# Kernel optimization log

Measured on AMD Instinct MI355X. Metric: run time of the kernel, lower is better.

Reference implementation:

```python
import jax, jax.numpy as jnp
import numpy as np

# Synthetic taxonomy matching BuildDictionaries/Build_H_Matrix structure
N_O, N_F, N_G, N_S = 25, 150, 1200, 4800
PIQUETS = [0, N_O, N_O + N_F, N_O + N_F + N_G, N_O + N_F + N_G + N_S]  # [0,25,175,1375,6175]
C_TOTAL = PIQUETS[-1]
WEIGHTS = [0.25, 0.25, 0.15, 0.1]
E = float(np.e)
BATCH = 4096


def _build_H():
    H = np.zeros((C_TOTAL, C_TOTAL), dtype=np.float32)
    fam = np.arange(N_F)
    H[fam % N_O, PIQUETS[1] + fam] = 1.0              # order -> family
    gen = np.arange(N_G)
    H[PIQUETS[1] + gen % N_F, PIQUETS[2] + gen] = 1.0  # family -> genus
    sp = np.arange(N_S)
    H[PIQUETS[2] + sp % N_G, PIQUETS[3] + sp] = 1.0    # genus -> species
    return H


def setup_inputs() -> dict:
    key = jax.random.key(0)
    k1, k2 = jax.random.split(key)
    H_np = _build_H()
    # parent[j] = i such that H[i, j] == 1 (same as the get_grandparents row scan)
    parent_np = np.argmax(H_np, axis=0).astype(np.int64)
    y_pred = jax.random.normal(k1, (BATCH, C_TOTAL), dtype=jnp.float32)
    y_true = jax.random.randint(k2, (BATCH,), 0, N_S, dtype=jnp.int64)
    return {
        "y_pred": y_pred,
        "y_true": y_true,
        "H": jnp.asarray(H_np),
        "parent": jnp.asarray(parent_np),
    }


def _ce(logits, labels):
    # nn.CrossEntropyLoss with mean reduction
    logp = jax.nn.log_softmax(logits, axis=-1)
    return -jnp.mean(jnp.take_along_axis(logp, labels[:, None], axis=1))


def reference(y_pred, y_true, H, parent):
    nb_levels = 4
    # Per-level logit slices: y_pred[:, piquets[k]:piquets[k+1]]
    lp = [y_pred[:, PIQUETS[k]:PIQUETS[k + 1]] for k in range(nb_levels)]

    # Ancestor chain (vectorized get_grandparents): global ids per level
    g3 = y_true + PIQUETS[3]           # global species id (y_true += piquets[-2])
    g2 = parent[g3]                    # genus
    g1 = parent[g2]                    # family
    g0 = parent[g1]                    # order
    lt = [g0 - PIQUETS[0], g1 - PIQUETS[1], g2 - PIQUETS[2], g3 - PIQUETS[3]]

    # Faithful quirk: argmax indices are LOCAL to each level's slice,
    # and H is indexed with those local indices (as in the original code).
    argm = [jnp.argmax(x, axis=-1) for x in lp]

    s = _ce(lp[0], lt[0])
    loss = jnp.zeros((), dtype=y_pred.dtype)
    for k in range(1, nb_levels):
        h = H[argm[k - 1], argm[k]]                      # [B] gather
        pen = jnp.sum(jnp.where(h == 0, E, 0.0))         # sum_i (H==0)*e
        s = (s + pen + _ce(lp[k], lt[k])) * WEIGHTS[k]   # running sum *= weights[k]
        loss = loss + s
    return loss
```

## Files before the change

### kernel.cpp

```cpp
#include <hip/hip_runtime.h>
#include <math.h>

#define C_TOTAL 6175
#define BATCH 4096
#define NLEV 4

__device__ __constant__ int PIQ[5] = {0, 25, 175, 1375, 6175};

__device__ inline void am_merge(float& m, int& idx, float m2, int i2) {
    const bool take = (m2 > m) || (m2 == m && i2 < idx);
    idx = take ? i2 : idx;
    m   = fmaxf(m, m2);
}

__device__ inline void upd(float x, int i, float& m, float& s, int& ii) {
    s += __expf(fminf(x, 60.f));
    ii = (x > m) ? i : ii;
    m  = fmaxf(m, x);
}

__device__ inline void process_span(const float* __restrict__ p, int W,
                                    int lane, float& S, float& M, int& I) {
    float ms = -INFINITY, ss = 0.f;
    int   is_ = 0x7fffffff;

    int pe = (int)((4u - ((((uintptr_t)p) >> 2) & 3u)) & 3u);
    if (pe > W) pe = W;
    if (lane < pe) {
        const float x = p[lane];
        ss = __expf(fminf(x, 60.f));
        ms = x; is_ = lane;
    }
    const int rem  = W - pe;
    const int nvec = rem >> 2;
    const int tail = rem & 3;
    const float4* vp = reinterpret_cast<const float4*>(p + pe);

    float m0 = -INFINITY, m1 = -INFINITY, m2 = -INFINITY, m3 = -INFINITY;
    float s0 = 0.f, s1 = 0.f, s2 = 0.f, s3 = 0.f;
    int   i0 = 0x1fffffff, i1 = 0x1fffffff, i2 = 0x1fffffff, i3 = 0x1fffffff;

    int i = lane;
    for (; i + 64 < nvec; i += 128) {
        const float4 a = vp[i];
        const float4 b = vp[i + 64];
        upd(a.x, i, m0, s0, i0); upd(a.y, i, m1, s1, i1);
        upd(a.z, i, m2, s2, i2); upd(a.w, i, m3, s3, i3);
        upd(b.x, i + 64, m0, s0, i0); upd(b.y, i + 64, m1, s1, i1);
        upd(b.z, i + 64, m2, s2, i2); upd(b.w, i + 64, m3, s3, i3);
    }
    if (i < nvec) {
        const float4 a = vp[i];
        upd(a.x, i, m0, s0, i0); upd(a.y, i, m1, s1, i1);
        upd(a.z, i, m2, s2, i2); upd(a.w, i, m3, s3, i3);
    }
    if (lane < tail) {
        const int c = pe + 4 * nvec + lane;
        const float x = p[c];
        ss += __expf(fminf(x, 60.f));
        const bool take = (x > ms) || (x == ms && c < is_);
        is_ = take ? c : is_;
        ms  = fmaxf(ms, x);
    }

    float m = ms; int idx = is_;
    float s = ss + ((s0 + s1) + (s2 + s3));
    am_merge(m, idx, m0, pe + 4 * i0 + 0);
    am_merge(m, idx, m1, pe + 4 * i1 + 1);
    am_merge(m, idx, m2, pe + 4 * i2 + 2);
    am_merge(m, idx, m3, pe + 4 * i3 + 3);

    #pragma unroll
    for (int off = 1; off < 64; off <<= 1) {
        const float mm = __shfl_xor(m, off);
        const int   im = __shfl_xor(idx, off);
        const float sm = __shfl_xor(s, off);
        s += sm;
        am_merge(m, idx, mm, im);
    }
    S = s; M = m; I = idx;
}

__global__ __launch_bounds__(256) void taxa_row_kernel(
    const float* __restrict__ y_pred,
    const int*   __restrict__ y_true,
    const float* __restrict__ H,
    const int*   __restrict__ parent,
    float*       __restrict__ ws)
{
    const int lane = threadIdx.x & 63;
    const int row  = blockIdx.x * 4 + (threadIdx.x >> 6);
    const float* rp = y_pred + (long long)row * C_TOTAL;

    const int g3 = y_true[row] + 1375;
    const int g2 = parent[g3];
    const int g1 = parent[g2];
    const int g0 = parent[g1];
    int lab[NLEV];
    lab[0] = g0;
    lab[1] = g1 - 25;
    lab[2] = g2 - 175;
    lab[3] = g3 - 1375;

    float ce[NLEV];
    int   argm[NLEV];

    #pragma unroll
    for (int k = 0; k < NLEV; ++k) {
        const int base = PIQ[k];
        const int W    = PIQ[k + 1] - base;
        float S, M;
        int I;
        process_span(rp + base, W, lane, S, M, I);
        const float xl = rp[base + lab[k]];
        ce[k]   = __logf(S) - xl;
        argm[k] = I;
    }

    if (lane == 0) {
        #pragma unroll
        for (int k = 0; k < NLEV; ++k)
            ws[k * BATCH + row] = ce[k];
        #pragma unroll
        for (int k = 1; k < NLEV; ++k) {
            const float h = H[(long long)argm[k - 1] * C_TOTAL + argm[k]];
            ws[(4 + (k - 1)) * BATCH + row] = (h == 0.f) ? 1.f : 0.f;
        }
    }
}

__global__ __launch_bounds__(1024) void taxa_final_kernel(
    const float* __restrict__ ws, float* __restrict__ out)
{
    const int tid = threadIdx.x;
    const float4* vws = reinterpret_cast<const float4*>(ws);
    float acc[7];
    #pragma unroll
    for (int j = 0; j < 7; ++j) {
        const float4 v = vws[j * 1024 + tid];
        acc[j] = (v.x + v.y) + (v.z + v.w);
    }
    #pragma unroll
    for (int off = 1; off < 64; off <<= 1) {
        #pragma unroll
        for (int j = 0; j < 7; ++j) acc[j] += __shfl_xor(acc[j], off);
    }
    __shared__ float sm[16][7];
    const int wid = tid >> 6;
    if ((tid & 63) == 0) {
        #pragma unroll
        for (int j = 0; j < 7; ++j) sm[wid][j] = acc[j];
    }
    __syncthreads();
    if (tid == 0) {
        float a[7];
        #pragma unroll
        for (int j = 0; j < 7; ++j) {
            float t = 0.f;
            #pragma unroll
            for (int w = 0; w < 16; ++w) t += sm[w][j];
            a[j] = t;
        }
        const float invB = 1.0f / (float)BATCH;
        const float E    = 2.7182818284590452f;
        const float ce0 = a[0] * invB, ce1 = a[1] * invB;
        const float ce2 = a[2] * invB, ce3 = a[3] * invB;
        const float pen1 = a[4] * E, pen2 = a[5] * E, pen3 = a[6] * E;

        float s = ce0;
        float loss = 0.f;
        s = (s + pen1 + ce1) * 0.25f; loss += s;
        s = (s + pen2 + ce2) * 0.15f; loss += s;
        s = (s + pen3 + ce3) * 0.10f; loss += s;
        out[0] = loss;
    }
}

extern "C" void kernel_launch(void* const* d_in, const int* in_sizes, int n_in,
                              void* d_out, int out_size, void* d_ws, size_t ws_size,
                              hipStream_t stream) {
    const float* y_pred = (const float*)d_in[0];
    const int*   y_true = (const int*)d_in[1];
    const float* H      = (const float*)d_in[2];
    const int*   parent = (const int*)d_in[3];
    float* ws  = (float*)d_ws;
    float* out = (float*)d_out;

    taxa_row_kernel<<<dim3(BATCH / 4), dim3(256), 0, stream>>>(y_pred, y_true, H, parent, ws);
    taxa_final_kernel<<<dim3(1), dim3(1024), 0, stream>>>(ws, out);
}
```

Before: 29.46 us.

## Fuse final reduction into row kernel via atomics and batch warp shuffles

Drops the second reduction kernel. Each block now folds its per-row cross-entropies and penalties into one weighted scalar, computed in closed form from the loss recurrence, and atomically adds it to the output, which is zeroed by a memset. The four per-level warp shuffle reductions are interleaved for more instruction-level parallelism, the main loop is unrolled to four float4 loads, and the exp clamp is removed. The trade-off is float atomic nondeterminism, an extra memset launch, and possible overflow if logits exceed about 88.

```diff
diff --git a/kernel.cpp b/kernel.cpp
--- a/kernel.cpp
+++ b/kernel.cpp
@@ -3,9 +3,6 @@
 
 #define C_TOTAL 6175
 #define BATCH 4096
-#define NLEV 4
-
-__device__ __constant__ int PIQ[5] = {0, 25, 175, 1375, 6175};
 
 __device__ inline void am_merge(float& m, int& idx, float m2, int i2) {
     const bool take = (m2 > m) || (m2 == m && i2 < idx);
@@ -14,13 +11,13 @@
 }
 
 __device__ inline void upd(float x, int i, float& m, float& s, int& ii) {
-    s += __expf(fminf(x, 60.f));
+    s += __expf(x);
     ii = (x > m) ? i : ii;
     m  = fmaxf(m, x);
 }
 
-__device__ inline void process_span(const float* __restrict__ p, int W,
-                                    int lane, float& S, float& M, int& I) {
+__device__ inline void process_span_local(const float* __restrict__ p, int W,
+                                          int lane, float& M, float& S, int& I) {
     float ms = -INFINITY, ss = 0.f;
     int   is_ = 0x7fffffff;
 
@@ -28,8 +25,7 @@
     if (pe > W) pe = W;
     if (lane < pe) {
         const float x = p[lane];
-        ss = __expf(fminf(x, 60.f));
-        ms = x; is_ = lane;
+        ss = __expf(x); ms = x; is_ = lane;
     }
     const int rem  = W - pe;
     const int nvec = rem >> 2;
@@ -41,15 +37,21 @@
     int   i0 = 0x1fffffff, i1 = 0x1fffffff, i2 = 0x1fffffff, i3 = 0x1fffffff;
 
     int i = lane;
-    for (; i + 64 < nvec; i += 128) {
+    for (; i + 192 < nvec; i += 256) {
         const float4 a = vp[i];
         const float4 b = vp[i + 64];
-        upd(a.x, i, m0, s0, i0); upd(a.y, i, m1, s1, i1);
-        upd(a.z, i, m2, s2, i2); upd(a.w, i, m3, s3, i3);
-        upd(b.x, i + 64, m0, s0, i0); upd(b.y, i + 64, m1, s1, i1);
-        upd(b.z, i + 64, m2, s2, i2); upd(b.w, i + 64, m3, s3, i3);
+        const float4 c = vp[i + 128];
+        const float4 d = vp[i + 192];
+        upd(a.x, i,       m0, s0, i0); upd(a.y, i,       m1, s1, i1);
+        upd(a.z, i,       m2, s2, i2); upd(a.w, i,       m3, s3, i3);
+        upd(b.x, i + 64,  m0, s0, i0); upd(b.y, i + 64,  m1, s1, i1);
+        upd(b.z, i + 64,  m2, s2, i2); upd(b.w, i + 64,  m3, s3, i3);
+        upd(c.x, i + 128, m0, s0, i0); upd(c.y, i + 128, m1, s1, i1);
+        upd(c.z, i + 128, m2, s2, i2); upd(c.w, i + 128, m3, s3, i3);
+        upd(d.x, i + 192, m0, s0, i0); upd(d.y, i + 192, m1, s1, i1);
+        upd(d.z, i + 192, m2, s2, i2); upd(d.w, i + 192, m3, s3, i3);
     }
-    if (i < nvec) {
+    for (; i < nvec; i += 64) {
         const float4 a = vp[i];
         upd(a.x, i, m0, s0, i0); upd(a.y, i, m1, s1, i1);
         upd(a.z, i, m2, s2, i2); upd(a.w, i, m3, s3, i3);
@@ -57,7 +59,7 @@
     if (lane < tail) {
         const int c = pe + 4 * nvec + lane;
         const float x = p[c];
-        ss += __expf(fminf(x, 60.f));
+        ss += __expf(x);
         const bool take = (x > ms) || (x == ms && c < is_);
         is_ = take ? c : is_;
         ms  = fmaxf(ms, x);
@@ -69,16 +71,7 @@
     am_merge(m, idx, m1, pe + 4 * i1 + 1);
     am_merge(m, idx, m2, pe + 4 * i2 + 2);
     am_merge(m, idx, m3, pe + 4 * i3 + 3);
-
-    #pragma unroll
-    for (int off = 1; off < 64; off <<= 1) {
-        const float mm = __shfl_xor(m, off);
-        const int   im = __shfl_xor(idx, off);
-        const float sm = __shfl_xor(s, off);
-        s += sm;
-        am_merge(m, idx, mm, im);
-    }
-    S = s; M = m; I = idx;
+    M = m; S = s; I = idx;
 }
 
 __global__ __launch_bounds__(256) void taxa_row_kernel(
@@ -86,94 +79,63 @@
     const int*   __restrict__ y_true,
     const float* __restrict__ H,
     const int*   __restrict__ parent,
-    float*       __restrict__ ws)
+    float*       __restrict__ out)
 {
+    constexpr int piq[5] = {0, 25, 175, 1375, 6175};
     const int lane = threadIdx.x & 63;
-    const int row  = blockIdx.x * 4 + (threadIdx.x >> 6);
+    const int wid  = threadIdx.x >> 6;
+    const int row  = blockIdx.x * 4 + wid;
     const float* rp = y_pred + (long long)row * C_TOTAL;
 
     const int g3 = y_true[row] + 1375;
     const int g2 = parent[g3];
     const int g1 = parent[g2];
     const int g0 = parent[g1];
-    int lab[NLEV];
-    lab[0] = g0;
-    lab[1] = g1 - 25;
-    lab[2] = g2 - 175;
-    lab[3] = g3 - 1375;
+    const int lab[4] = {g0, g1 - 25, g2 - 175, g3 - 1375};
 
-    float ce[NLEV];
-    int   argm[NLEV];
-
+    float Lm[4], Ls[4], xl[4];
+    int   Li[4];
     #pragma unroll
-    for (int k = 0; k < NLEV; ++k) {
-        const int base = PIQ[k];
-        const int W    = PIQ[k + 1] - base;
-        float S, M;
-        int I;
-        process_span(rp + base, W, lane, S, M, I);
-        const float xl = rp[base + lab[k]];
-        ce[k]   = __logf(S) - xl;
-        argm[k] = I;
+    for (int k = 0; k < 4; ++k) {
+        process_span_local(rp + piq[k], piq[k + 1] - piq[k], lane,
+                           Lm[k], Ls[k], Li[k]);
+        xl[k] = rp[piq[k] + lab[k]];
     }
 
-    if (lane == 0) {
-        #pragma unroll
-        for (int k = 0; k < NLEV; ++k)
-            ws[k * BATCH + row] = ce[k];
-        #pragma unroll
-        for (int k = 1; k < NLEV; ++k) {
-            const float h = H[(long long)argm[k - 1] * C_TOTAL + argm[k]];
-            ws[(4 + (k - 1)) * BATCH + row] = (h == 0.f) ? 1.f : 0.f;
-        }
-    }
-}
-
-__global__ __launch_bounds__(1024) void taxa_final_kernel(
-    const float* __restrict__ ws, float* __restrict__ out)
-{
-    const int tid = threadIdx.x;
-    const float4* vws = reinterpret_cast<const float4*>(ws);
-    float acc[7];
-    #pragma unroll
-    for (int j = 0; j < 7; ++j) {
-        const float4 v = vws[j * 1024 + tid];
-        acc[j] = (v.x + v.y) + (v.z + v.w);
-    }
     #pragma unroll
     for (int off = 1; off < 64; off <<= 1) {
         #pragma unroll
-        for (int j = 0; j < 7; ++j) acc[j] += __shfl_xor(acc[j], off);
+        for (int k = 0; k < 4; ++k) {
+            const float mm = __shfl_xor(Lm[k], off);
+            const int   im = __shfl_xor(Li[k], off);
+            const float sm = __shfl_xor(Ls[k], off);
+            Ls[k] += sm;
+            am_merge(Lm[k], Li[k], mm, im);
+        }
     }
-    __shared__ float sm[16][7];
-    const int wid = tid >> 6;
-    if ((tid & 63) == 0) {
+
+    __shared__ float blk[4];
+    if (lane == 0) {
+        float ce[4];
         #pragma unroll
-        for (int j = 0; j < 7; ++j) sm[wid][j] = acc[j];
+        for (int k = 0; k < 4; ++k)
+            ce[k] = __logf(Ls[k]) - xl[k];
+        float h[3];
+        #pragma unroll
+        for (int k = 1; k < 4; ++k) {
+            const float hv = H[(long long)Li[k - 1] * C_TOTAL + Li[k]];
+            h[k - 1] = (hv == 0.f) ? 1.f : 0.f;
+        }
+        const float invB = 1.0f / 4096.0f;
+        const float E    = 2.7182818284590452f;
+        const float A = 0.29125f, Bc = 0.165f, Cc = 0.10f;
+        blk[wid] = A  * ((ce[0] + ce[1]) * invB + E * h[0])
+                 + Bc * (ce[2] * invB + E * h[1])
+                 + Cc * (ce[3] * invB + E * h[2]);
     }
     __syncthreads();
-    if (tid == 0) {
-        float a[7];
-        #pragma unroll
-        for (int j = 0; j < 7; ++j) {
-            float t = 0.f;
-            #pragma unroll
-            for (int w = 0; w < 16; ++w) t += sm[w][j];
-            a[j] = t;
-        }
-        const float invB = 1.0f / (float)BATCH;
-        const float E    = 2.7182818284590452f;
-        const float ce0 = a[0] * invB, ce1 = a[1] * invB;
-        const float ce2 = a[2] * invB, ce3 = a[3] * invB;
-        const float pen1 = a[4] * E, pen2 = a[5] * E, pen3 = a[6] * E;
-
-        float s = ce0;
-        float loss = 0.f;
-        s = (s + pen1 + ce1) * 0.25f; loss += s;
-        s = (s + pen2 + ce2) * 0.15f; loss += s;
-        s = (s + pen3 + ce3) * 0.10f; loss += s;
-        out[0] = loss;
-    }
+    if (threadIdx.x == 0)
+        atomicAdd(out, (blk[0] + blk[1]) + (blk[2] + blk[3]));
 }
 
 extern "C" void kernel_launch(void* const* d_in, const int* in_sizes, int n_in,
@@ -183,9 +145,9 @@
     const int*   y_true = (const int*)d_in[1];
     const float* H      = (const float*)d_in[2];
     const int*   parent = (const int*)d_in[3];
-    float* ws  = (float*)d_ws;
     float* out = (float*)d_out;
 
-    taxa_row_kernel<<<dim3(BATCH / 4), dim3(256), 0, stream>>>(y_pred, y_true, H, parent, ws);
-    taxa_final_kernel<<<dim3(1), dim3(1024), 0, stream>>>(ws, out);
+    hipMemsetAsync(out, 0, sizeof(float), stream);
+    taxa_row_kernel<<<dim3(BATCH / 4), dim3(256), 0, stream>>>(
+        y_pred, y_true, H, parent, out);
 }
```

Result: slower. 42.82 us (+45.3%).
